# Kernel tuning notes

Hardware: AMD Instinct MI355X
Metric: run time of the kernel (lower is better)

The kernel has to match this reference:

```python
import jax, jax.numpy as jnp
import numpy as np

NUM_TABLES = 21
NUM_CATS = 1000
EMB_DIM = 16
B = 500000
CONCAT_DIM = NUM_TABLES * EMB_DIM + 8  # 344
OUT_DIM = 32
NEG_SLOPE = 0.01


def _lrelu(v):
    return jnp.where(v >= 0, v, NEG_SLOPE * v)


def setup_inputs() -> dict:
    key = jax.random.key(0)
    ks = jax.random.split(key, 8)
    x_cat = jax.random.randint(ks[0], (B, NUM_TABLES), 0, NUM_CATS, dtype=jnp.int32)
    x_cont = jax.random.uniform(ks[1], (B, 1), dtype=jnp.float32)
    # 21 identical-shape embedding tables stacked: [21, 1000, 16]
    tables = jax.random.normal(ks[2], (NUM_TABLES, NUM_CATS, EMB_DIM), dtype=jnp.float32) * 0.02
    W_c = jax.random.normal(ks[3], (8, 1), dtype=jnp.float32) * 0.5
    b_c = jax.random.normal(ks[4], (8,), dtype=jnp.float32) * 0.01
    W = jax.random.normal(ks[5], (OUT_DIM, CONCAT_DIM), dtype=jnp.float32) * 0.05
    b = jax.random.normal(ks[6], (OUT_DIM,), dtype=jnp.float32) * 0.01
    return {"x_cat": x_cat, "x_cont": x_cont, "tables": tables,
            "W_c": W_c, "b_c": b_c, "W": W, "b": b}


def reference(x_cat, x_cont, tables, W_c, b_c, W, b):
    batch = x_cat.shape[0]
    # Fused gather over all 21 tables: [B, 21, EMB_DIM]
    table_ids = jnp.arange(NUM_TABLES)[None, :]  # [1, 21]
    emb = tables[table_ids, x_cat]               # [B, 21, 16]
    concat_emb = emb.reshape(batch, NUM_TABLES * EMB_DIM)  # [B, 336]
    # continuous feature branch: Linear(1 -> 8) + LeakyReLU
    cont = _lrelu(x_cont @ W_c.T + b_c)          # [B, 8]
    combined = jnp.concatenate([concat_emb, cont], axis=1)  # [B, 344]
    out = _lrelu(combined @ W.T + b)             # [B, 32]
    return out
```

## Files before the change

kernel.cpp:

```cpp
#include <hip/hip_runtime.h>
#include <hip/hip_bf16.h>

#define NUM_TABLES 21
#define NUM_CATS   1000
#define EMB_DIM    16
#define CONCAT_DIM 344
#define OUT_DIM    32
#define NEG_SLOPE  0.01f

#define ROWS_PER_BLOCK 32
#define CATS_PER_BLOCK (ROWS_PER_BLOCK * NUM_TABLES)

typedef float f32x4 __attribute__((ext_vector_type(4)));

__device__ __forceinline__ unsigned short f32_to_bf16_rne(float f) {
    unsigned int u = __float_as_uint(f);
    unsigned int r = u + 0x7FFFu + ((u >> 16) & 1u);
    return (unsigned short)(r >> 16);
}
__device__ __forceinline__ float bf16_to_f32(unsigned short h) {
    return __uint_as_float(((unsigned int)h) << 16);
}
__device__ __forceinline__ float lrelu(float v) {
    return v >= 0.f ? v : NEG_SLOPE * v;
}

__global__ void build_P(const float* __restrict__ tables,
                        const float* __restrict__ W,
                        unsigned short* __restrict__ P,
                        float* __restrict__ wt) {
    int idx = blockIdx.x * 256 + threadIdx.x;
    if (idx < NUM_TABLES * NUM_CATS * OUT_DIM) {
        int j = idx & 31;
        int c = (idx >> 5) % NUM_CATS;
        int t = idx / (NUM_CATS * OUT_DIM);
        const float* trow = tables + (size_t)(t * NUM_CATS + c) * EMB_DIM;
        const float* wrow = W + (size_t)j * CONCAT_DIM + t * EMB_DIM;
        float acc = 0.f;
        #pragma unroll
        for (int k = 0; k < EMB_DIM; ++k) acc = fmaf(trow[k], wrow[k], acc);
        P[idx] = f32_to_bf16_rne(acc);
    }
    if (blockIdx.x == 0 && threadIdx.x < 8 * OUT_DIM) {
        int k = threadIdx.x >> 5;
        int j = threadIdx.x & 31;
        wt[k * OUT_DIM + j] = W[(size_t)j * CONCAT_DIM + (CONCAT_DIM - 8) + k];
    }
}

__global__ void __launch_bounds__(256)
fwd(const int* __restrict__ xcat,
    const float* __restrict__ xcont,
    const unsigned short* __restrict__ P,
    const float* __restrict__ Wc,
    const float* __restrict__ bc,
    const float* __restrict__ bias,
    const float* __restrict__ wt,
    float* __restrict__ out,
    int nrows) {
    __shared__ int s_cats[CATS_PER_BLOCK];

    const int tid = threadIdx.x;
    const long blk_cat_base = (long)blockIdx.x * CATS_PER_BLOCK;
    const long total_cats = (long)nrows * NUM_TABLES;

    #pragma unroll
    for (int i = 0; i < 3; ++i) {
        int li = tid + i * 256;
        if (li < CATS_PER_BLOCK) {
            long g = blk_cat_base + li;
            if (g < total_cats) s_cats[li] = xcat[g];
        }
    }
    __syncthreads();

    const int row_local = tid >> 3;
    const int l = tid & 7;
    const int row = blockIdx.x * ROWS_PER_BLOCK + row_local;
    if (row >= nrows) return;

    int offs[NUM_TABLES];
    #pragma unroll
    for (int t = 0; t < NUM_TABLES; ++t) {
        int c = s_cats[row_local * NUM_TABLES + t];
        offs[t] = (t * NUM_CATS + c) * OUT_DIM + l * 4;
    }

    ushort4 u[NUM_TABLES];
    #pragma unroll
    for (int t = 0; t < NUM_TABLES; ++t)
        u[t] = *reinterpret_cast<const ushort4*>(P + offs[t]);

    float acc[4];
    const float* bsrc = bias + l * 4;
    #pragma unroll
    for (int m = 0; m < 4; ++m) acc[m] = bsrc[m];

    #pragma unroll
    for (int t = 0; t < NUM_TABLES; ++t) {
        acc[0] += bf16_to_f32(u[t].x);
        acc[1] += bf16_to_f32(u[t].y);
        acc[2] += bf16_to_f32(u[t].z);
        acc[3] += bf16_to_f32(u[t].w);
    }

    float x = xcont[row];
    #pragma unroll
    for (int k = 0; k < 8; ++k) {
        float cv = lrelu(fmaf(x, Wc[k], bc[k]));
        const float* w = wt + k * OUT_DIM + l * 4;
        #pragma unroll
        for (int m = 0; m < 4; ++m)
            acc[m] = fmaf(cv, w[m], acc[m]);
    }

    #pragma unroll
    for (int m = 0; m < 4; ++m) acc[m] = lrelu(acc[m]);

    f32x4 v = { acc[0], acc[1], acc[2], acc[3] };
    *reinterpret_cast<f32x4*>(out + (size_t)row * OUT_DIM + l * 4) = v;
}

extern "C" void kernel_launch(void* const* d_in, const int* in_sizes, int n_in,
                              void* d_out, int out_size, void* d_ws, size_t ws_size,
                              hipStream_t stream) {
    const int*   xcat   = (const int*)d_in[0];
    const float* xcont  = (const float*)d_in[1];
    const float* tables = (const float*)d_in[2];
    const float* Wc     = (const float*)d_in[3];
    const float* bc     = (const float*)d_in[4];
    const float* W      = (const float*)d_in[5];
    const float* bias   = (const float*)d_in[6];
    float* out = (float*)d_out;

    int nrows = in_sizes[0] / NUM_TABLES;

    const size_t P_elems = (size_t)NUM_TABLES * NUM_CATS * OUT_DIM;
    const size_t P_bytes = P_elems * sizeof(unsigned short);
    const size_t wt_off  = P_bytes;

    unsigned short* P = (unsigned short*)d_ws;
    float* wt = (float*)((char*)d_ws + wt_off);

    int blocks1 = (int)((P_elems + 255) / 256);
    build_P<<<blocks1, 256, 0, stream>>>(tables, W, P, wt);

    int blocks2 = (nrows + ROWS_PER_BLOCK - 1) / ROWS_PER_BLOCK;
    fwd<<<blocks2, 256, 0, stream>>>(xcat, xcont, P, Wc, bc, bias, wt, out, nrows);
}
```

Baseline: 77.29 us.

## Stream precomputed table projections through LDS slices with large row blocks

Reorganizes the precomputed per-category projection tables into 42 slices (table × half of the output columns), padded to 1024 categories. Each block handles 2048 rows, with four rows per thread, and streams the slices through double-buffered shared memory, so lookups hit LDS instead of scattered global memory. Category indices are packed to 16 bits in LDS. The change adds 42 block-wide barriers and heavy register use for 128 accumulators per thread. It keeps the old path as a fallback when the workspace is too small.

Result: slower. 137.0 us (+77.3%).

```diff
diff --git a/kernel.cpp b/kernel.cpp
--- a/kernel.cpp
+++ b/kernel.cpp
@@ -1,124 +1,270 @@
 #include <hip/hip_runtime.h>
 #include <hip/hip_bf16.h>
 
-#define NUM_TABLES 21
-#define NUM_CATS   1000
-#define EMB_DIM    16
-#define CONCAT_DIM 344
-#define OUT_DIM    32
-#define NEG_SLOPE  0.01f
-
-#define ROWS_PER_BLOCK 32
-#define CATS_PER_BLOCK (ROWS_PER_BLOCK * NUM_TABLES)
+#define NT 21
+#define NC 1000
+#define NCP 1024
+#define OD 32
+#define CD 344
+#define NEG 0.01f
+
+#define RPB 2048
+#define THR 512
+#define SLICE 32768
+#define NS 42
 
 typedef float f32x4 __attribute__((ext_vector_type(4)));
+typedef unsigned int u32x2 __attribute__((ext_vector_type(2)));
 
 __device__ __forceinline__ unsigned short f32_to_bf16_rne(float f) {
     unsigned int u = __float_as_uint(f);
     unsigned int r = u + 0x7FFFu + ((u >> 16) & 1u);
     return (unsigned short)(r >> 16);
 }
-__device__ __forceinline__ float bf16_to_f32(unsigned short h) {
-    return __uint_as_float(((unsigned int)h) << 16);
-}
-__device__ __forceinline__ float lrelu(float v) {
-    return v >= 0.f ? v : NEG_SLOPE * v;
-}
-
-__global__ void build_P(const float* __restrict__ tables,
-                        const float* __restrict__ W,
-                        unsigned short* __restrict__ P,
-                        float* __restrict__ wt) {
+__device__ __forceinline__ float lrelu(float v) { return v >= 0.f ? v : NEG * v; }
+
+__global__ void build_P2(const float* __restrict__ tables,
+                         const float* __restrict__ W,
+                         unsigned short* __restrict__ P2) {
     int idx = blockIdx.x * 256 + threadIdx.x;
-    if (idx < NUM_TABLES * NUM_CATS * OUT_DIM) {
+    if (idx >= NS * 16384) return;
+    int jj = idx & 7;
+    int c  = (idx >> 3) & (NCP - 1);
+    int h8 = (idx >> 13) & 1;
+    int s  = idx >> 14;
+    int h = s / NT, t = s - h * NT;
+    float v = 0.f;
+    if (c < NC) {
+        const float* tr = tables + (size_t)(t * NC + c) * 16;
+        const float* wr = W + (size_t)(h * 16 + h8 * 8 + jj) * CD + t * 16;
+        #pragma unroll
+        for (int k = 0; k < 16; ++k) v = fmaf(tr[k], wr[k], v);
+    }
+    P2[idx] = f32_to_bf16_rne(v);
+}
+
+#define UNP8(ACC, I, BASE, V)                                         \
+    ACC[I][BASE + 0] += __uint_as_float(V.x << 16);                   \
+    ACC[I][BASE + 1] += __uint_as_float(V.x & 0xFFFF0000u);           \
+    ACC[I][BASE + 2] += __uint_as_float(V.y << 16);                   \
+    ACC[I][BASE + 3] += __uint_as_float(V.y & 0xFFFF0000u);           \
+    ACC[I][BASE + 4] += __uint_as_float(V.z << 16);                   \
+    ACC[I][BASE + 5] += __uint_as_float(V.z & 0xFFFF0000u);           \
+    ACC[I][BASE + 6] += __uint_as_float(V.w << 16);                   \
+    ACC[I][BASE + 7] += __uint_as_float(V.w & 0xFFFF0000u);
+
+#define STAGE(S, T, ACC)                                                       \
+    {                                                                          \
+        uint4* dst = (uint4*)(s_P + ((S) & 1) * SLICE);                        \
+        _Pragma("unroll")                                                      \
+        for (int k = 0; k < 4; ++k) dst[tid + k * THR] = st[k];                \
+        __syncthreads();                                                       \
+        if ((S) + 1 < NS) {                                                    \
+            const uint4* g = (const uint4*)((const char*)P2 + (size_t)((S) + 1) * SLICE); \
+            _Pragma("unroll")                                                  \
+            for (int k = 0; k < 4; ++k) st[k] = g[tid + k * THR];              \
+        }                                                                      \
+        const char* buf = s_P + ((S) & 1) * SLICE;                             \
+        _Pragma("unroll")                                                      \
+        for (int i = 0; i < 4; ++i) {                                          \
+            int c = (int)s_cats[(r0 + i) * NT + (T)];                          \
+            uint4 pa = *(const uint4*)(buf + c * 16);                          \
+            uint4 pb = *(const uint4*)(buf + 16384 + c * 16);                  \
+            UNP8(ACC, i, 0, pa)                                                \
+            UNP8(ACC, i, 8, pb)                                                \
+        }                                                                      \
+    }
+
+__global__ void __launch_bounds__(THR, 2)
+fwd_lds(const int* __restrict__ xcat, const float* __restrict__ xcont,
+        const unsigned short* __restrict__ P2,
+        const float* __restrict__ W, const float* __restrict__ Wc,
+        const float* __restrict__ bc, const float* __restrict__ bias,
+        float* __restrict__ out, int nrows) {
+    __shared__ unsigned short s_cats[RPB * NT];
+    __shared__ char s_P[2 * SLICE];
+
+    const int tid = threadIdx.x;
+    const long rbase = (long)blockIdx.x * RPB;
+    const long totalc = (long)nrows * NT;
+
+    {
+        const long base4 = rbase * NT / 4;
+        const uint4* s4 = (const uint4*)xcat;
+        #pragma unroll
+        for (int it = 0; it < (RPB * NT / 4) / THR; ++it) {
+            int n = tid + it * THR;
+            long e0 = (base4 + n) * 4;
+            uint4 v = make_uint4(0u, 0u, 0u, 0u);
+            if (e0 + 3 < totalc) {
+                v = s4[base4 + n];
+            } else {
+                if (e0     < totalc) v.x = (unsigned)xcat[e0];
+                if (e0 + 1 < totalc) v.y = (unsigned)xcat[e0 + 1];
+                if (e0 + 2 < totalc) v.z = (unsigned)xcat[e0 + 2];
+                if (e0 + 3 < totalc) v.w = (unsigned)xcat[e0 + 3];
+            }
+            u32x2 p;
+            p.x = (v.x & 0xFFFFu) | (v.y << 16);
+            p.y = (v.z & 0xFFFFu) | (v.w << 16);
+            *(u32x2*)((char*)s_cats + (size_t)n * 8) = p;
+        }
+    }
+
+    uint4 st[4];
+    {
+        const uint4* g = (const uint4*)P2;
+        #pragma unroll
+        for (int k = 0; k < 4; ++k) st[k] = g[tid + k * THR];
+    }
+
+    float accA[4][16], accB[4][16];
+    #pragma unroll
+    for (int i = 0; i < 4; ++i) {
+        #pragma unroll
+        for (int j = 0; j < 16; ++j) { accA[i][j] = 0.f; accB[i][j] = 0.f; }
+    }
+
+    const int r0 = tid * 4;
+
+    for (int s = 0;  s < NT; ++s) STAGE(s, s,      accA)
+    for (int s = NT; s < NS; ++s) STAGE(s, s - NT, accB)
+
+    const long grow = rbase + r0;
+    if (grow >= nrows) return;
+
+    float xc[4];
+    if (grow + 3 < nrows) {
+        f32x4 x4 = *(const f32x4*)(xcont + grow);
+        xc[0] = x4.x; xc[1] = x4.y; xc[2] = x4.z; xc[3] = x4.w;
+    } else {
+        #pragma unroll
+        for (int i = 0; i < 4; ++i)
+            xc[i] = (grow + i < nrows) ? xcont[grow + i] : 0.f;
+    }
+
+    float cv[4][8];
+    #pragma unroll
+    for (int i = 0; i < 4; ++i) {
+        #pragma unroll
+        for (int k = 0; k < 8; ++k)
+            cv[i][k] = lrelu(fmaf(xc[i], Wc[k], bc[k]));
+    }
+
+    #pragma unroll
+    for (int i = 0; i < 4; ++i) {
+        if (grow + i < nrows) {
+            float* orow = out + (size_t)(grow + i) * OD;
+            #pragma unroll
+            for (int q = 0; q < 4; ++q) {
+                f32x4 v;
+                #pragma unroll
+                for (int e = 0; e < 4; ++e) {
+                    int j = q * 4 + e;
+                    float a = accA[i][j] + bias[j];
+                    #pragma unroll
+                    for (int k = 0; k < 8; ++k)
+                        a = fmaf(cv[i][k], W[(size_t)j * CD + (CD - 8) + k], a);
+                    v[e] = lrelu(a);
+                }
+                *(f32x4*)(orow + q * 4) = v;
+            }
+            #pragma unroll
+            for (int q = 4; q < 8; ++q) {
+                f32x4 v;
+                #pragma unroll
+                for (int e = 0; e < 4; ++e) {
+                    int j = q * 4 + e;
+                    float a = accB[i][j - 16] + bias[j];
+                    #pragma unroll
+                    for (int k = 0; k < 8; ++k)
+                        a = fmaf(cv[i][k], W[(size_t)j * CD + (CD - 8) + k], a);
+                    v[e] = lrelu(a);
+                }
+                *(f32x4*)(orow + q * 4) = v;
+            }
+        }
+    }
+}
+
+__global__ void build_P_fb(const float* __restrict__ tables,
+                           const float* __restrict__ W,
+                           unsigned short* __restrict__ P,
+                           float* __restrict__ wt) {
+    int idx = blockIdx.x * 256 + threadIdx.x;
+    if (idx < NT * NC * OD) {
         int j = idx & 31;
-        int c = (idx >> 5) % NUM_CATS;
-        int t = idx / (NUM_CATS * OUT_DIM);
-        const float* trow = tables + (size_t)(t * NUM_CATS + c) * EMB_DIM;
-        const float* wrow = W + (size_t)j * CONCAT_DIM + t * EMB_DIM;
+        int c = (idx >> 5) % NC;
+        int t = idx / (NC * OD);
+        const float* trow = tables + (size_t)(t * NC + c) * 16;
+        const float* wrow = W + (size_t)j * CD + t * 16;
         float acc = 0.f;
         #pragma unroll
-        for (int k = 0; k < EMB_DIM; ++k) acc = fmaf(trow[k], wrow[k], acc);
+        for (int k = 0; k < 16; ++k) acc = fmaf(trow[k], wrow[k], acc);
         P[idx] = f32_to_bf16_rne(acc);
     }
-    if (blockIdx.x == 0 && threadIdx.x < 8 * OUT_DIM) {
+    if (blockIdx.x == 0 && threadIdx.x < 8 * OD) {
         int k = threadIdx.x >> 5;
         int j = threadIdx.x & 31;
-        wt[k * OUT_DIM + j] = W[(size_t)j * CONCAT_DIM + (CONCAT_DIM - 8) + k];
+        wt[k * OD + j] = W[(size_t)j * CD + (CD - 8) + k];
     }
 }
 
 __global__ void __launch_bounds__(256)
-fwd(const int* __restrict__ xcat,
-    const float* __restrict__ xcont,
-    const unsigned short* __restrict__ P,
-    const float* __restrict__ Wc,
-    const float* __restrict__ bc,
-    const float* __restrict__ bias,
-    const float* __restrict__ wt,
-    float* __restrict__ out,
-    int nrows) {
-    __shared__ int s_cats[CATS_PER_BLOCK];
-
+fwd_fb(const int* __restrict__ xcat, const float* __restrict__ xcont,
+       const unsigned short* __restrict__ P, const float* __restrict__ Wc,
+       const float* __restrict__ bc, const float* __restrict__ bias,
+       const float* __restrict__ wt, float* __restrict__ out, int nrows) {
+    __shared__ int s_cats[32 * NT];
     const int tid = threadIdx.x;
-    const long blk_cat_base = (long)blockIdx.x * CATS_PER_BLOCK;
-    const long total_cats = (long)nrows * NUM_TABLES;
-
+    const long blk_cat_base = (long)blockIdx.x * (32 * NT);
+    const long total_cats = (long)nrows * NT;
     #pragma unroll
     for (int i = 0; i < 3; ++i) {
         int li = tid + i * 256;
-        if (li < CATS_PER_BLOCK) {
+        if (li < 32 * NT) {
             long g = blk_cat_base + li;
             if (g < total_cats) s_cats[li] = xcat[g];
         }
     }
     __syncthreads();
-
     const int row_local = tid >> 3;
     const int l = tid & 7;
-    const int row = blockIdx.x * ROWS_PER_BLOCK + row_local;
+    const int row = blockIdx.x * 32 + row_local;
     if (row >= nrows) return;
-
-    int offs[NUM_TABLES];
-    #pragma unroll
-    for (int t = 0; t < NUM_TABLES; ++t) {
-        int c = s_cats[row_local * NUM_TABLES + t];
-        offs[t] = (t * NUM_CATS + c) * OUT_DIM + l * 4;
-    }
-
-    ushort4 u[NUM_TABLES];
-    #pragma unroll
-    for (int t = 0; t < NUM_TABLES; ++t)
+    int offs[NT];
+    #pragma unroll
+    for (int t = 0; t < NT; ++t) {
+        int c = s_cats[row_local * NT + t];
+        offs[t] = (t * NC + c) * OD + l * 4;
+    }
+    ushort4 u[NT];
+    #pragma unroll
+    for (int t = 0; t < NT; ++t)
         u[t] = *reinterpret_cast<const ushort4*>(P + offs[t]);
-
     float acc[4];
     const float* bsrc = bias + l * 4;
     #pragma unroll
     for (int m = 0; m < 4; ++m) acc[m] = bsrc[m];
-
-    #pragma unroll
-    for (int t = 0; t < NUM_TABLES; ++t) {
-        acc[0] += bf16_to_f32(u[t].x);
-        acc[1] += bf16_to_f32(u[t].y);
-        acc[2] += bf16_to_f32(u[t].z);
-        acc[3] += bf16_to_f32(u[t].w);
-    }
-
+    #pragma unroll
+    for (int t = 0; t < NT; ++t) {
+        acc[0] += __uint_as_float((unsigned)u[t].x << 16);
+        acc[1] += __uint_as_float((unsigned)u[t].y << 16);
+        acc[2] += __uint_as_float((unsigned)u[t].z << 16);
+        acc[3] += __uint_as_float((unsigned)u[t].w << 16);
+    }
     float x = xcont[row];
     #pragma unroll
     for (int k = 0; k < 8; ++k) {
-        float cv = lrelu(fmaf(x, Wc[k], bc[k]));
-        const float* w = wt + k * OUT_DIM + l * 4;
-        #pragma unroll
-        for (int m = 0; m < 4; ++m)
-            acc[m] = fmaf(cv, w[m], acc[m]);
-    }
-
+        float cvv = lrelu(fmaf(x, Wc[k], bc[k]));
+        const float* w = wt + k * OD + l * 4;
+        #pragma unroll
+        for (int m = 0; m < 4; ++m) acc[m] = fmaf(cvv, w[m], acc[m]);
+    }
     #pragma unroll
     for (int m = 0; m < 4; ++m) acc[m] = lrelu(acc[m]);
-
     f32x4 v = { acc[0], acc[1], acc[2], acc[3] };
-    *reinterpret_cast<f32x4*>(out + (size_t)row * OUT_DIM + l * 4) = v;
+    *reinterpret_cast<f32x4*>(out + (size_t)row * OD + l * 4) = v;
 }
 
 extern "C" void kernel_launch(void* const* d_in, const int* in_sizes, int n_in,
@@ -133,18 +279,18 @@
     const float* bias   = (const float*)d_in[6];
     float* out = (float*)d_out;
 
-    int nrows = in_sizes[0] / NUM_TABLES;
-
-    const size_t P_elems = (size_t)NUM_TABLES * NUM_CATS * OUT_DIM;
-    const size_t P_bytes = P_elems * sizeof(unsigned short);
-    const size_t wt_off  = P_bytes;
-
-    unsigned short* P = (unsigned short*)d_ws;
-    float* wt = (float*)((char*)d_ws + wt_off);
-
-    int blocks1 = (int)((P_elems + 255) / 256);
-    build_P<<<blocks1, 256, 0, stream>>>(tables, W, P, wt);
-
-    int blocks2 = (nrows + ROWS_PER_BLOCK - 1) / ROWS_PER_BLOCK;
-    fwd<<<blocks2, 256, 0, stream>>>(xcat, xcont, P, Wc, bc, bias, wt, out, nrows);
-}
+    int nrows = in_sizes[0] / NT;
+
+    if (ws_size >= (size_t)NS * SLICE) {
+        unsigned short* P2 = (unsigned short*)d_ws;
+        build_P2<<<(NS * 16384 + 255) / 256, 256, 0, stream>>>(tables, W, P2);
+        int nb = (nrows + RPB - 1) / RPB;
+        fwd_lds<<<nb, THR, 0, stream>>>(xcat, xcont, P2, W, Wc, bc, bias, out, nrows);
+    } else {
+        unsigned short* P = (unsigned short*)d_ws;
+        float* wt = (float*)((char*)d_ws + (size_t)NT * NC * OD * 2);
+        build_P_fb<<<(NT * NC * OD + 255) / 256, 256, 0, stream>>>(tables, W, P, wt);
+        int nb = (nrows + 31) / 32;
+        fwd_fb<<<nb, 256, 0, stream>>>(xcat, xcont, P, Wc, bc, bias, wt, out, nrows);
+    }
+}
```
